# Optimization experiments

Measured on AMD Instinct MI355X. Metric: run time of the kernel, lower is better.

## Reference

```python
import jax, jax.numpy as jnp
import numpy as np
from jax.ops import segment_sum, segment_max

N, E = 50000, 800000
IN_FEATS, H, D_HID, N_CLASSES = 256, 4, 32, 47
NEG_SLOPE = 0.2


def leaky_relu(x, slope=NEG_SLOPE):
    return jnp.where(x >= 0, x, slope * x)


def gat_conv(h, W, attn_l, attn_r, src, dst, n_nodes, heads, d_out):
    # h: [N, F_in]; W: [F_in, heads*d_out]; attn_l/attn_r: [heads, d_out]
    feat = (h @ W).reshape(n_nodes, heads, d_out)          # [N, H, D]
    el = jnp.sum(feat * attn_l, axis=-1)                   # [N, H]
    er = jnp.sum(feat * attn_r, axis=-1)                   # [N, H]
    e = leaky_relu(el[src] + er[dst])                      # [E, H]
    # segment softmax over incoming edges of each dst node
    e_max = segment_max(e, dst, num_segments=n_nodes)      # [N, H]
    e_exp = jnp.exp(e - e_max[dst])                        # [E, H]
    denom = segment_sum(e_exp, dst, num_segments=n_nodes)  # [N, H]
    alpha = e_exp / denom[dst]                             # [E, H]
    msg = feat[src] * alpha[..., None]                     # [E, H, D]
    return segment_sum(msg, dst, num_segments=n_nodes)     # [N, H, D]


def setup_inputs() -> dict:
    key = jax.random.key(0)
    ks = jax.random.split(key, 12)
    hd = H * D_HID
    def glorot(k, shape):
        fan = shape[0] + shape[-1] if len(shape) == 2 else int(np.prod(shape))
        return jax.random.normal(k, shape, dtype=jnp.float32) * np.sqrt(2.0 / fan)
    return {
        "x": jax.random.normal(ks[0], (N, IN_FEATS), dtype=jnp.float32),
        "src": jax.random.randint(ks[1], (E,), 0, N),
        "dst": jax.random.randint(ks[2], (E,), 0, N),
        "W1": glorot(ks[3], (IN_FEATS, hd)),
        "al1": glorot(ks[4], (H, D_HID)),
        "ar1": glorot(ks[5], (H, D_HID)),
        "W2": glorot(ks[6], (hd, hd)),
        "al2": glorot(ks[7], (H, D_HID)),
        "ar2": glorot(ks[8], (H, D_HID)),
        "W3": glorot(ks[9], (hd, H * N_CLASSES)),
        "al3": glorot(ks[10], (H, N_CLASSES)),
        "ar3": glorot(ks[11], (H, N_CLASSES)),
    }


def reference(x, src, dst, W1, al1, ar1, W2, al2, ar2, W3, al3, ar3):
    # layer 1: ELU activation, flatten heads
    h = gat_conv(x, W1, al1, ar1, src, dst, N, H, D_HID)
    h = jax.nn.elu(h).reshape(N, H * D_HID)
    # layer 2
    h = gat_conv(h, W2, al2, ar2, src, dst, N, H, D_HID)
    h = jax.nn.elu(h).reshape(N, H * D_HID)
    # layer 3: no activation, mean over heads, log softmax
    h = gat_conv(h, W3, al3, ar3, src, dst, N, H, N_CLASSES)
    h = h.mean(axis=1)                                      # [N, n_classes]
    return jax.nn.log_softmax(h, axis=-1)
```

## Files before the change

kernel.cpp:

```cpp
#include <hip/hip_runtime.h>
#include <hip/hip_bf16.h>
#include <math.h>
#include <string.h>

#define N_NODES 50000
#define N_EDGES 800000
#define NH 4

typedef unsigned int u32;
typedef unsigned short u16;
typedef __attribute__((ext_vector_type(8))) short bf16x8;
typedef __attribute__((ext_vector_type(4))) float f32x4;

__device__ __forceinline__ u32 pack_bf2(float a, float b) {
    __hip_bfloat162 h2 = __float22bfloat162_rn(make_float2(a, b));
    u32 r;
    memcpy(&r, &h2, 4);
    return r;
}
__device__ __forceinline__ float2 bf2_to_f2(u32 u) {
    return make_float2(__uint_as_float(u << 16), __uint_as_float(u & 0xffff0000u));
}
__device__ __forceinline__ short bf16r(float f) {
    __hip_bfloat16 h = __float2bfloat16(f);
    short s;
    memcpy(&s, &h, 2);
    return s;
}

__device__ __forceinline__ float wred_max(float v) {
#pragma unroll
    for (int o = 32; o > 0; o >>= 1) v = fmaxf(v, __shfl_xor(v, o));
    return v;
}
__device__ __forceinline__ float wred_sum(float v) {
#pragma unroll
    for (int o = 32; o > 0; o >>= 1) v += __shfl_xor(v, o);
    return v;
}


__global__ void k_hist(const int* __restrict__ dst, int* __restrict__ deg) {
    int i = blockIdx.x * 256 + threadIdx.x;
    if (i < N_EDGES) atomicAdd(&deg[dst[i]], 1);
}

__global__ __launch_bounds__(1024) void k_scan1(const int* __restrict__ deg,
                                                int* __restrict__ offs,
                                                int* __restrict__ bsum) {
    __shared__ int tmp[1024];
    int b = blockIdx.x, t = threadIdx.x;
    int i = b * 1024 + t;
    int v = (i < N_NODES) ? deg[i] : 0;
    tmp[t] = v;
    __syncthreads();
    for (int off = 1; off < 1024; off <<= 1) {
        int add = (t >= off) ? tmp[t - off] : 0;
        __syncthreads();
        tmp[t] += add;
        __syncthreads();
    }
    if (i < N_NODES) offs[i] = tmp[t] - v;
    if (t == 1023) bsum[b] = tmp[t];
}

__global__ void k_scan2(int* __restrict__ bsum, int nb) {
    if (blockIdx.x == 0 && threadIdx.x == 0) {
        int run = 0;
        for (int b = 0; b < nb; ++b) { int v = bsum[b]; bsum[b] = run; run += v; }
    }
}

__global__ __launch_bounds__(1024) void k_scan3(int* __restrict__ offs,
                                                const int* __restrict__ bsum,
                                                int* __restrict__ cursor) {
    int b = blockIdx.x, t = threadIdx.x;
    int i = b * 1024 + t;
    if (i < N_NODES) {
        int o = offs[i] + bsum[b];
        offs[i] = o;
        cursor[i] = o;
    }
    if (b == 0 && t == 0) offs[N_NODES] = N_EDGES;
}

__global__ void k_scatter(const int* __restrict__ src, const int* __restrict__ dst,
                          int* __restrict__ cursor, int* __restrict__ csrc) {
    int i = blockIdx.x * 256 + threadIdx.x;
    if (i < N_EDGES) {
        int p = atomicAdd(&cursor[dst[i]], 1);
        csrc[p] = src[i];
    }
}

template <int K, int NOUT, int NP>
__global__ void prep_w(const float* __restrict__ W, u16* __restrict__ Wp) {
    constexpr int NT = NP / 16;
    int idx = blockIdx.x * 256 + threadIdx.x;
    int total = (K / 32) * NT * 64 * 8;
    if (idx >= total) return;
    int j = idx & 7;
    int lane = (idx >> 3) & 63;
    int rest = idx >> 9;
    int nt = rest % NT;
    int kt = rest / NT;
    int k = kt * 32 + (lane >> 4) * 8 + j;
    int col = nt * 16 + (lane & 15);
    float v = (col < NOUT) ? W[(size_t)k * NOUT + col] : 0.f;
    Wp[idx] = (u16)bf16r(v);
}

template <int K>
__global__ void prep_w3(const float* __restrict__ W, u16* __restrict__ Wp) {
    constexpr int NT = 12;
    int idx = blockIdx.x * 256 + threadIdx.x;
    int total = (K / 32) * NT * 64 * 8;
    if (idx >= total) return;
    int j = idx & 7;
    int lane = (idx >> 3) & 63;
    int rest = idx >> 9;
    int nt = rest % NT;
    int kt = rest / NT;
    int k = kt * 32 + (lane >> 4) * 8 + j;
    int col = nt * 16 + (lane & 15);
    int h = col / 48, d = col % 48;
    float v = (d < 47) ? W[(size_t)k * 188 + h * 47 + d] : 0.f;
    Wp[idx] = (u16)bf16r(v);
}

template <int K, int NOUT, int NP, bool AF32, bool DOTS, bool HEADPAD>
__global__ __launch_bounds__(256) void gemm_mfma(const void* __restrict__ Av,
                                                 const u16* __restrict__ Wp,
                                                 u16* __restrict__ feat,
                                                 const float* __restrict__ al,
                                                 const float* __restrict__ ar,
                                                 float* __restrict__ el,
                                                 float* __restrict__ er) {
    constexpr int NT = NP / 16;
    constexpr int KT = K / 32;
    int w = threadIdx.x >> 6, l = threadIdx.x & 63;
    int tile_m0 = blockIdx.x * 64 + w * 16;
    int c15 = l & 15;
    int rowA = tile_m0 + c15;
    if (rowA >= N_NODES) rowA = N_NODES - 1;
    int g = l >> 4;

    f32x4 acc[NT];
#pragma unroll
    for (int nt = 0; nt < NT; ++nt) acc[nt] = (f32x4){0.f, 0.f, 0.f, 0.f};

    for (int kt = 0; kt < KT; ++kt) {
        bf16x8 a;
        if constexpr (AF32) {
            const float* ap = (const float*)Av + (size_t)rowA * K + kt * 32 + g * 8;
            float4 f0 = *reinterpret_cast<const float4*>(ap);
            float4 f1 = *reinterpret_cast<const float4*>(ap + 4);
            a[0] = bf16r(f0.x); a[1] = bf16r(f0.y); a[2] = bf16r(f0.z); a[3] = bf16r(f0.w);
            a[4] = bf16r(f1.x); a[5] = bf16r(f1.y); a[6] = bf16r(f1.z); a[7] = bf16r(f1.w);
        } else {
            a = *reinterpret_cast<const bf16x8*>((const u16*)Av + (size_t)rowA * K + kt * 32 + g * 8);
        }
        const u16* wp = Wp + ((size_t)kt * NT) * 512 + (size_t)l * 8;
#pragma unroll
        for (int nt = 0; nt < NT; ++nt) {
            bf16x8 b = *reinterpret_cast<const bf16x8*>(wp + nt * 512);
            acc[nt] = __builtin_amdgcn_mfma_f32_16x16x32_bf16(a, b, acc[nt], 0, 0, 0);
        }
    }

    int rowD0 = tile_m0 + g * 4;
#pragma unroll
    for (int nt = 0; nt < NT; ++nt) {
        int col = nt * 16 + c15;
#pragma unroll
        for (int r = 0; r < 4; ++r) {
            int row = rowD0 + r;
            if (row < N_NODES)
                feat[(size_t)row * NP + col] = (u16)bf16r(acc[nt][r]);
        }
    }

    if constexpr (DOTS) {
        float alv[NT], arv[NT];
#pragma unroll
        for (int nt = 0; nt < NT; ++nt) {
            if constexpr (HEADPAD) {
                int h = nt / 3, m = nt % 3;
                if (m == 2) {
                    alv[nt] = (c15 < 15) ? al[h * 47 + 32 + c15] : 0.f;
                    arv[nt] = (c15 < 15) ? ar[h * 47 + 32 + c15] : 0.f;
                } else {
                    alv[nt] = al[h * 47 + m * 16 + c15];
                    arv[nt] = ar[h * 47 + m * 16 + c15];
                }
            } else {
                alv[nt] = al[nt * 16 + c15];
                arv[nt] = ar[nt * 16 + c15];
            }
        }
#pragma unroll
        for (int r = 0; r < 4; ++r) {
            float hlv[NH] = {0.f, 0.f, 0.f, 0.f};
            float hrv[NH] = {0.f, 0.f, 0.f, 0.f};
#pragma unroll
            for (int nt = 0; nt < NT; ++nt) {
                constexpr int NTH = NT / NH;
                int h = nt / NTH;
                hlv[h] = fmaf(acc[nt][r], alv[nt], hlv[h]);
                hrv[h] = fmaf(acc[nt][r], arv[nt], hrv[h]);
            }
#pragma unroll
            for (int o = 1; o < 16; o <<= 1) {
#pragma unroll
                for (int j = 0; j < NH; ++j) {
                    hlv[j] += __shfl_xor(hlv[j], o);
                    hrv[j] += __shfl_xor(hrv[j], o);
                }
            }
            int row = rowD0 + r;
            if (c15 == 0 && row < N_NODES) {
                *reinterpret_cast<float4*>(el + (size_t)row * NH) =
                    make_float4(hlv[0], hlv[1], hlv[2], hlv[3]);
                *reinterpret_cast<float4*>(er + (size_t)row * NH) =
                    make_float4(hrv[0], hrv[1], hrv[2], hrv[3]);
            }
        }
    }
}

__device__ __forceinline__ void alpha_chunk_T(const float* __restrict__ el,
                                              const int* __restrict__ csrc,
                                              float4 erv, int base, int i1,
                                              float4 mref, float4 vinv, bool online,
                                              float* __restrict__ lalT,
                                              int* __restrict__ lsrc, int lane) {
    int e = base + lane;
    bool act = e < i1;
    int srcn = act ? csrc[e] : 0;
    float4 elv = make_float4(0.f, 0.f, 0.f, 0.f);
    if (act) elv = *reinterpret_cast<const float4*>(el + (size_t)srcn * NH);
    float e0 = elv.x + erv.x; e0 = e0 >= 0.f ? e0 : 0.2f * e0;
    float e1 = elv.y + erv.y; e1 = e1 >= 0.f ? e1 : 0.2f * e1;
    float e2 = elv.z + erv.z; e2 = e2 >= 0.f ? e2 : 0.2f * e2;
    float e3 = elv.w + erv.w; e3 = e3 >= 0.f ? e3 : 0.2f * e3;
    float4 a4;
    if (online) {
        const float NEG = -__builtin_inff();
        float f0 = act ? e0 : NEG, f1 = act ? e1 : NEG, f2 = act ? e2 : NEG, f3 = act ? e3 : NEG;
        float m0 = wred_max(f0), m1 = wred_max(f1), m2 = wred_max(f2), m3 = wred_max(f3);
        float p0 = act ? __expf(e0 - m0) : 0.f;
        float p1 = act ? __expf(e1 - m1) : 0.f;
        float p2 = act ? __expf(e2 - m2) : 0.f;
        float p3 = act ? __expf(e3 - m3) : 0.f;
        float s0 = wred_sum(p0), s1 = wred_sum(p1), s2 = wred_sum(p2), s3 = wred_sum(p3);
        a4 = make_float4(act ? p0 / s0 : 0.f, act ? p1 / s1 : 0.f,
                         act ? p2 / s2 : 0.f, act ? p3 / s3 : 0.f);
    } else {
        a4 = make_float4(act ? __expf(e0 - mref.x) * vinv.x : 0.f,
                         act ? __expf(e1 - mref.y) * vinv.y : 0.f,
                         act ? __expf(e2 - mref.z) * vinv.z : 0.f,
                         act ? __expf(e3 - mref.w) * vinv.w : 0.f);
    }
    lalT[0 * 64 + lane] = a4.x;
    lalT[1 * 64 + lane] = a4.y;
    lalT[2 * 64 + lane] = a4.z;
    lalT[3 * 64 + lane] = a4.w;
    lsrc[lane] = srcn;
}

__device__ __forceinline__ void stats_pass(const float* __restrict__ el,
                                           const int* __restrict__ csrc,
                                           float4 erv, int i0, int i1, int lane,
                                           float4& mout, float4& vout) {
    const float NEG = -__builtin_inff();
    float m0 = NEG, m1 = NEG, m2 = NEG, m3 = NEG;
    float s0 = 0.f, s1 = 0.f, s2 = 0.f, s3 = 0.f;
    for (int base = i0; base < i1; base += 64) {
        int i = base + lane;
        bool act = i < i1;
        int srcn = act ? csrc[i] : 0;
        float4 elv = make_float4(0.f, 0.f, 0.f, 0.f);
        if (act) elv = *reinterpret_cast<const float4*>(el + (size_t)srcn * NH);
        float e0 = elv.x + erv.x; e0 = e0 >= 0.f ? e0 : 0.2f * e0;
        float e1 = elv.y + erv.y; e1 = e1 >= 0.f ? e1 : 0.2f * e1;
        float e2 = elv.z + erv.z; e2 = e2 >= 0.f ? e2 : 0.2f * e2;
        float e3 = elv.w + erv.w; e3 = e3 >= 0.f ? e3 : 0.2f * e3;
        if (!act) { e0 = NEG; e1 = NEG; e2 = NEG; e3 = NEG; }
        float c0 = wred_max(e0), c1 = wred_max(e1), c2 = wred_max(e2), c3 = wred_max(e3);
        float nm0 = fmaxf(m0, c0), nm1 = fmaxf(m1, c1), nm2 = fmaxf(m2, c2), nm3 = fmaxf(m3, c3);
        float p0 = act ? __expf(e0 - nm0) : 0.f;
        float p1 = act ? __expf(e1 - nm1) : 0.f;
        float p2 = act ? __expf(e2 - nm2) : 0.f;
        float p3 = act ? __expf(e3 - nm3) : 0.f;
        float S0 = wred_sum(p0), S1 = wred_sum(p1), S2 = wred_sum(p2), S3 = wred_sum(p3);
        s0 = s0 * __expf(m0 - nm0) + S0; m0 = nm0;
        s1 = s1 * __expf(m1 - nm1) + S1; m1 = nm1;
        s2 = s2 * __expf(m2 - nm2) + S2; m2 = nm2;
        s3 = s3 * __expf(m3 - nm3) + S3; m3 = nm3;
    }
    mout = make_float4(m0, m1, m2, m3);
    vout = make_float4(1.f / s0, 1.f / s1, 1.f / s2, 1.f / s3);
}

__global__ __launch_bounds__(256) void gat_agg128(const u16* __restrict__ feat,
                                                  const float* __restrict__ el,
                                                  const float* __restrict__ er,
                                                  const int* __restrict__ offs,
                                                  const int* __restrict__ csrc,
                                                  u16* __restrict__ out) {
    __shared__ float lalT[4][4][64];
    __shared__ int lsrc[4][64];
    int wave = threadIdx.x >> 6;
    int lane = threadIdx.x & 63;
    int n = blockIdx.x * 4 + wave;
    int h = lane >> 4;
    int i0 = offs[n], i1 = offs[n + 1];
    int d = i1 - i0;
    float ax = 0.f, ay = 0.f;
    if (d > 0) {
        float4 erv = *reinterpret_cast<const float4*>(er + (size_t)n * NH);
        float4 mref = make_float4(0.f, 0.f, 0.f, 0.f), vinv = mref;
        bool onechunk = d <= 64;
        if (!onechunk) stats_pass(el, csrc, erv, i0, i1, lane, mref, vinv);
        for (int base = i0; base < i1; base += 64) {
            alpha_chunk_T(el, csrc, erv, base, i1, mref, vinv, onechunk,
                          &lalT[wave][0][0], &lsrc[wave][0], lane);
            int cnt = i1 - base; if (cnt > 64) cnt = 64;
            int cpad = (cnt + 3) & ~3;
            for (int j = 0; j < cpad; j += 4) {
                int4 sv = *reinterpret_cast<const int4*>(&lsrc[wave][j]);
                float4 aq = *reinterpret_cast<const float4*>(&lalT[wave][h][j]);
                u32 q0 = *reinterpret_cast<const u32*>(feat + (size_t)sv.x * 128 + 2 * lane);
                u32 q1 = *reinterpret_cast<const u32*>(feat + (size_t)sv.y * 128 + 2 * lane);
                u32 q2 = *reinterpret_cast<const u32*>(feat + (size_t)sv.z * 128 + 2 * lane);
                u32 q3 = *reinterpret_cast<const u32*>(feat + (size_t)sv.w * 128 + 2 * lane);
                float2 v;
                v = bf2_to_f2(q0); ax = fmaf(aq.x, v.x, ax); ay = fmaf(aq.x, v.y, ay);
                v = bf2_to_f2(q1); ax = fmaf(aq.y, v.x, ax); ay = fmaf(aq.y, v.y, ay);
                v = bf2_to_f2(q2); ax = fmaf(aq.z, v.x, ax); ay = fmaf(aq.z, v.y, ay);
                v = bf2_to_f2(q3); ax = fmaf(aq.w, v.x, ax); ay = fmaf(aq.w, v.y, ay);
            }
        }
    }
    float ox = ax > 0.f ? ax : expm1f(ax);
    float oy = ay > 0.f ? ay : expm1f(ay);
    *reinterpret_cast<u32*>(out + (size_t)n * 128 + 2 * lane) = pack_bf2(ox, oy);
}

__global__ __launch_bounds__(256) void gat_agg_final(const u16* __restrict__ feat,
                                                     const float* __restrict__ el,
                                                     const float* __restrict__ er,
                                                     const int* __restrict__ offs,
                                                     const int* __restrict__ csrc,
                                                     float* __restrict__ out) {
    __shared__ float lalT[4][4][64];
    __shared__ int lsrc[4][64];
    __shared__ float lds[4][192];
    int wave = threadIdx.x >> 6;
    int lane = threadIdx.x & 63;
    int n = blockIdx.x * 4 + wave;
    int e0 = 2 * lane;
    bool up = lane < 32;
    int hLo = e0 / 48;
    int hHi = up ? (128 + e0) / 48 : 3;
    int i0 = offs[n], i1 = offs[n + 1];
    int d = i1 - i0;
    float a00 = 0.f, a01 = 0.f, a10 = 0.f, a11 = 0.f;
    if (d > 0) {
        float4 erv = *reinterpret_cast<const float4*>(er + (size_t)n * NH);
        float4 mref = make_float4(0.f, 0.f, 0.f, 0.f), vinv = mref;
        bool onechunk = d <= 64;
        if (!onechunk) stats_pass(el, csrc, erv, i0, i1, lane, mref, vinv);
        for (int base = i0; base < i1; base += 64) {
            alpha_chunk_T(el, csrc, erv, base, i1, mref, vinv, onechunk,
                          &lalT[wave][0][0], &lsrc[wave][0], lane);
            int cnt = i1 - base; if (cnt > 64) cnt = 64;
            int cpad = (cnt + 3) & ~3;
            for (int j = 0; j < cpad; j += 4) {
                int4 sv = *reinterpret_cast<const int4*>(&lsrc[wave][j]);
                float4 wlo = *reinterpret_cast<const float4*>(&lalT[wave][hLo][j]);
                float4 whi = *reinterpret_cast<const float4*>(&lalT[wave][hHi][j]);
                const u16* rA = feat + (size_t)sv.x * 192;
                const u16* rB = feat + (size_t)sv.y * 192;
                const u16* rC = feat + (size_t)sv.z * 192;
                const u16* rD = feat + (size_t)sv.w * 192;
                u32 a0 = *reinterpret_cast<const u32*>(rA + e0);
                u32 b0 = *reinterpret_cast<const u32*>(rB + e0);
                u32 c0 = *reinterpret_cast<const u32*>(rC + e0);
                u32 d0 = *reinterpret_cast<const u32*>(rD + e0);
                u32 a1 = up ? *reinterpret_cast<const u32*>(rA + 128 + e0) : 0u;
                u32 b1 = up ? *reinterpret_cast<const u32*>(rB + 128 + e0) : 0u;
                u32 c1 = up ? *reinterpret_cast<const u32*>(rC + 128 + e0) : 0u;
                u32 d1 = up ? *reinterpret_cast<const u32*>(rD + 128 + e0) : 0u;
                float2 v;
                v = bf2_to_f2(a0); a00 = fmaf(wlo.x, v.x, a00); a01 = fmaf(wlo.x, v.y, a01);
                v = bf2_to_f2(b0); a00 = fmaf(wlo.y, v.x, a00); a01 = fmaf(wlo.y, v.y, a01);
                v = bf2_to_f2(c0); a00 = fmaf(wlo.z, v.x, a00); a01 = fmaf(wlo.z, v.y, a01);
                v = bf2_to_f2(d0); a00 = fmaf(wlo.w, v.x, a00); a01 = fmaf(wlo.w, v.y, a01);
                v = bf2_to_f2(a1); a10 = fmaf(whi.x, v.x, a10); a11 = fmaf(whi.x, v.y, a11);
                v = bf2_to_f2(b1); a10 = fmaf(whi.y, v.x, a10); a11 = fmaf(whi.y, v.y, a11);
                v = bf2_to_f2(c1); a10 = fmaf(whi.z, v.x, a10); a11 = fmaf(whi.z, v.y, a11);
                v = bf2_to_f2(d1); a10 = fmaf(whi.w, v.x, a10); a11 = fmaf(whi.w, v.y, a11);
            }
        }
    }
    lds[wave][e0] = a00;
    lds[wave][e0 + 1] = a01;
    if (up) {
        lds[wave][128 + e0] = a10;
        lds[wave][129 + e0] = a11;
    }
    __syncthreads();
    float u = (lane < 47)
                  ? 0.25f * (lds[wave][lane] + lds[wave][48 + lane] +
                             lds[wave][96 + lane] + lds[wave][144 + lane])
                  : -__builtin_inff();
    float mx = u;
#pragma unroll
    for (int o = 32; o > 0; o >>= 1) mx = fmaxf(mx, __shfl_xor(mx, o));
    float ex = (lane < 47) ? __expf(u - mx) : 0.f;
    float sm = ex;
#pragma unroll
    for (int o = 32; o > 0; o >>= 1) sm += __shfl_xor(sm, o);
    if (lane < 47) out[(size_t)n * 47 + lane] = u - mx - logf(sm);
}


extern "C" void kernel_launch(void* const* d_in, const int* in_sizes, int n_in,
                              void* d_out, int out_size, void* d_ws, size_t ws_size,
                              hipStream_t stream) {
    const float* x = (const float*)d_in[0];
    const int* src = (const int*)d_in[1];
    const int* dst = (const int*)d_in[2];
    const float* W1 = (const float*)d_in[3];
    const float* al1 = (const float*)d_in[4];
    const float* ar1 = (const float*)d_in[5];
    const float* W2 = (const float*)d_in[6];
    const float* al2 = (const float*)d_in[7];
    const float* ar2 = (const float*)d_in[8];
    const float* W3 = (const float*)d_in[9];
    const float* al3 = (const float*)d_in[10];
    const float* ar3 = (const float*)d_in[11];
    float* out = (float*)d_out;

    char* p = (char*)d_ws;
    auto alloc = [&](size_t bytes) {
        char* r = p;
        p += (bytes + 255) & ~(size_t)255;
        return r;
    };
    u16* bufA = (u16*)alloc((size_t)N_NODES * 128 * 2);
    u16* bufC = (u16*)alloc((size_t)N_NODES * 128 * 2);
    u16* featb = (u16*)alloc((size_t)N_NODES * 192 * 2);
    float* el = (float*)alloc((size_t)N_NODES * NH * 4);
    float* er = (float*)alloc((size_t)N_NODES * NH * 4);
    u16* wp1 = (u16*)alloc((size_t)(256 / 32) * 8 * 512 * 2);
    u16* wp2 = (u16*)alloc((size_t)(128 / 32) * 8 * 512 * 2);
    u16* wp3 = (u16*)alloc((size_t)(128 / 32) * 12 * 512 * 2);
    int* deg = (int*)alloc((size_t)N_NODES * 4);
    int* offs = (int*)alloc((size_t)(N_NODES + 1) * 4);
    int* cursor = (int*)alloc((size_t)N_NODES * 4);
    int* bsum = (int*)alloc(64 * 4);
    int* csrc = (int*)alloc((size_t)N_EDGES * 4);

    prep_w<256, 128, 128><<<(8 * 8 * 512 + 255) / 256, 256, 0, stream>>>(W1, wp1);
    prep_w<128, 128, 128><<<(4 * 8 * 512 + 255) / 256, 256, 0, stream>>>(W2, wp2);
    prep_w3<128><<<(4 * 12 * 512 + 255) / 256, 256, 0, stream>>>(W3, wp3);

    hipMemsetAsync(deg, 0, (size_t)N_NODES * 4, stream);
    k_hist<<<(N_EDGES + 255) / 256, 256, 0, stream>>>(dst, deg);
    k_scan1<<<49, 1024, 0, stream>>>(deg, offs, bsum);
    k_scan2<<<1, 64, 0, stream>>>(bsum, 49);
    k_scan3<<<49, 1024, 0, stream>>>(offs, bsum, cursor);
    k_scatter<<<(N_EDGES + 255) / 256, 256, 0, stream>>>(src, dst, cursor, csrc);

    int gemm_grid = (N_NODES + 63) / 64;
    gemm_mfma<256, 128, 128, true, true, false><<<gemm_grid, 256, 0, stream>>>(x, wp1, featb, al1, ar1, el, er);
    gat_agg128<<<N_NODES / 4, 256, 0, stream>>>(featb, el, er, offs, csrc, bufA);
    gemm_mfma<128, 128, 128, false, true, false><<<gemm_grid, 256, 0, stream>>>(bufA, wp2, featb, al2, ar2, el, er);
    gat_agg128<<<N_NODES / 4, 256, 0, stream>>>(featb, el, er, offs, csrc, bufC);
    gemm_mfma<128, 192, 192, false, true, true><<<gemm_grid, 256, 0, stream>>>(bufC, wp3, featb, al3, ar3, el, er);
    gat_agg_final<<<N_NODES / 4, 256, 0, stream>>>(featb, el, er, offs, csrc, out);
}
```

Measured before the change: 314.1 us.

## Merge weight-prep kernels, warp-scan block sums, and use packed FMA in aggregation

Merges the three weight-packing kernels into a single launch and replaces the serial single-thread block-sum scan with a wavefront shuffle scan. The aggregation kernels now store each attention weight twice in a padded LDS layout, so v_pk_fma_f32 can apply one weight to both bf16-unpacked feature lanes at once. The goal is fewer launches, a shorter serial scan, and half as many FMA instructions in the gather loops. In exchange, LDS attention reads double and inline asm may limit compiler scheduling.

Measured after the change: 302.8 us. 3.6% less time.

```diff
diff --git a/kernel.cpp b/kernel.cpp
--- a/kernel.cpp
+++ b/kernel.cpp
@@ -6,11 +6,13 @@
 #define N_NODES 50000
 #define N_EDGES 800000
 #define NH 4
+#define LSTR 136
 
 typedef unsigned int u32;
 typedef unsigned short u16;
 typedef __attribute__((ext_vector_type(8))) short bf16x8;
 typedef __attribute__((ext_vector_type(4))) float f32x4;
+typedef __attribute__((ext_vector_type(2))) float f32x2;
 
 __device__ __forceinline__ u32 pack_bf2(float a, float b) {
     __hip_bfloat162 h2 = __float22bfloat162_rn(make_float2(a, b));
@@ -18,14 +20,20 @@
     memcpy(&r, &h2, 4);
     return r;
 }
-__device__ __forceinline__ float2 bf2_to_f2(u32 u) {
-    return make_float2(__uint_as_float(u << 16), __uint_as_float(u & 0xffff0000u));
+__device__ __forceinline__ f32x2 bf2_to_v2(u32 u) {
+    f32x2 v;
+    v.x = __uint_as_float(u << 16);
+    v.y = __uint_as_float(u & 0xffff0000u);
+    return v;
 }
 __device__ __forceinline__ short bf16r(float f) {
     __hip_bfloat16 h = __float2bfloat16(f);
     short s;
     memcpy(&s, &h, 2);
     return s;
+}
+__device__ __forceinline__ void pkfma(f32x2& acc, f32x2 a, f32x2 b) {
+    asm("v_pk_fma_f32 %0, %1, %2, %0" : "+v"(acc) : "v"(a), "v"(b));
 }
 
 __device__ __forceinline__ float wred_max(float v) {
@@ -65,10 +73,15 @@
 }
 
 __global__ void k_scan2(int* __restrict__ bsum, int nb) {
-    if (blockIdx.x == 0 && threadIdx.x == 0) {
-        int run = 0;
-        for (int b = 0; b < nb; ++b) { int v = bsum[b]; bsum[b] = run; run += v; }
-    }
+    int t = threadIdx.x & 63;
+    int v = (t < nb) ? bsum[t] : 0;
+    int orig = v;
+#pragma unroll
+    for (int o = 1; o < 64; o <<= 1) {
+        int u = __shfl_up(v, o);
+        if (t >= o) v += u;
+    }
+    if (t < nb) bsum[t] = v - orig;
 }
 
 __global__ __launch_bounds__(1024) void k_scan3(int* __restrict__ offs,
@@ -93,39 +106,42 @@
     }
 }
 
-template <int K, int NOUT, int NP>
-__global__ void prep_w(const float* __restrict__ W, u16* __restrict__ Wp) {
-    constexpr int NT = NP / 16;
-    int idx = blockIdx.x * 256 + threadIdx.x;
-    int total = (K / 32) * NT * 64 * 8;
-    if (idx >= total) return;
-    int j = idx & 7;
-    int lane = (idx >> 3) & 63;
-    int rest = idx >> 9;
+__device__ __forceinline__ u16 pack_elem(const float* W, int i, int K, int NT, int NOUT) {
+    int j = i & 7;
+    int lane = (i >> 3) & 63;
+    int rest = i >> 9;
     int nt = rest % NT;
     int kt = rest / NT;
     int k = kt * 32 + (lane >> 4) * 8 + j;
     int col = nt * 16 + (lane & 15);
     float v = (col < NOUT) ? W[(size_t)k * NOUT + col] : 0.f;
-    Wp[idx] = (u16)bf16r(v);
-}
-
-template <int K>
-__global__ void prep_w3(const float* __restrict__ W, u16* __restrict__ Wp) {
-    constexpr int NT = 12;
-    int idx = blockIdx.x * 256 + threadIdx.x;
-    int total = (K / 32) * NT * 64 * 8;
-    if (idx >= total) return;
-    int j = idx & 7;
-    int lane = (idx >> 3) & 63;
-    int rest = idx >> 9;
-    int nt = rest % NT;
-    int kt = rest / NT;
+    return (u16)bf16r(v);
+}
+__device__ __forceinline__ u16 pack_elem3(const float* W, int i) {
+    int j = i & 7;
+    int lane = (i >> 3) & 63;
+    int rest = i >> 9;
+    int nt = rest % 12;
+    int kt = rest / 12;
     int k = kt * 32 + (lane >> 4) * 8 + j;
     int col = nt * 16 + (lane & 15);
     int h = col / 48, d = col % 48;
     float v = (d < 47) ? W[(size_t)k * 188 + h * 47 + d] : 0.f;
-    Wp[idx] = (u16)bf16r(v);
+    return (u16)bf16r(v);
+}
+__global__ void prep_all(const float* __restrict__ W1, const float* __restrict__ W2,
+                         const float* __restrict__ W3, u16* __restrict__ wp1,
+                         u16* __restrict__ wp2, u16* __restrict__ wp3) {
+    int idx = blockIdx.x * 256 + threadIdx.x;
+    if (idx < 32768) {
+        wp1[idx] = pack_elem(W1, idx, 256, 8, 128);
+    } else if (idx < 49152) {
+        int i = idx - 32768;
+        wp2[i] = pack_elem(W2, i, 128, 8, 128);
+    } else if (idx < 73728) {
+        int i = idx - 49152;
+        wp3[i] = pack_elem3(W3, i);
+    }
 }
 
 template <int K, int NOUT, int NP, bool AF32, bool DOTS, bool HEADPAD>
@@ -261,10 +277,10 @@
                          act ? __expf(e2 - mref.z) * vinv.z : 0.f,
                          act ? __expf(e3 - mref.w) * vinv.w : 0.f);
     }
-    lalT[0 * 64 + lane] = a4.x;
-    lalT[1 * 64 + lane] = a4.y;
-    lalT[2 * 64 + lane] = a4.z;
-    lalT[3 * 64 + lane] = a4.w;
+    *reinterpret_cast<f32x2*>(&lalT[0 * LSTR + 2 * lane]) = (f32x2){a4.x, a4.x};
+    *reinterpret_cast<f32x2*>(&lalT[1 * LSTR + 2 * lane]) = (f32x2){a4.y, a4.y};
+    *reinterpret_cast<f32x2*>(&lalT[2 * LSTR + 2 * lane]) = (f32x2){a4.z, a4.z};
+    *reinterpret_cast<f32x2*>(&lalT[3 * LSTR + 2 * lane]) = (f32x2){a4.w, a4.w};
     lsrc[lane] = srcn;
 }
 
@@ -308,7 +324,7 @@
                                                   const int* __restrict__ offs,
                                                   const int* __restrict__ csrc,
                                                   u16* __restrict__ out) {
-    __shared__ float lalT[4][4][64];
+    __shared__ float lalT[4][4][LSTR];
     __shared__ int lsrc[4][64];
     int wave = threadIdx.x >> 6;
     int lane = threadIdx.x & 63;
@@ -316,7 +332,7 @@
     int h = lane >> 4;
     int i0 = offs[n], i1 = offs[n + 1];
     int d = i1 - i0;
-    float ax = 0.f, ay = 0.f;
+    f32x2 acc = (f32x2){0.f, 0.f};
     if (d > 0) {
         float4 erv = *reinterpret_cast<const float4*>(er + (size_t)n * NH);
         float4 mref = make_float4(0.f, 0.f, 0.f, 0.f), vinv = mref;
@@ -329,21 +345,25 @@
             int cpad = (cnt + 3) & ~3;
             for (int j = 0; j < cpad; j += 4) {
                 int4 sv = *reinterpret_cast<const int4*>(&lsrc[wave][j]);
-                float4 aq = *reinterpret_cast<const float4*>(&lalT[wave][h][j]);
-                u32 q0 = *reinterpret_cast<const u32*>(feat + (size_t)sv.x * 128 + 2 * lane);
-                u32 q1 = *reinterpret_cast<const u32*>(feat + (size_t)sv.y * 128 + 2 * lane);
-                u32 q2 = *reinterpret_cast<const u32*>(feat + (size_t)sv.z * 128 + 2 * lane);
-                u32 q3 = *reinterpret_cast<const u32*>(feat + (size_t)sv.w * 128 + 2 * lane);
-                float2 v;
-                v = bf2_to_f2(q0); ax = fmaf(aq.x, v.x, ax); ay = fmaf(aq.x, v.y, ay);
-                v = bf2_to_f2(q1); ax = fmaf(aq.y, v.x, ax); ay = fmaf(aq.y, v.y, ay);
-                v = bf2_to_f2(q2); ax = fmaf(aq.z, v.x, ax); ay = fmaf(aq.z, v.y, ay);
-                v = bf2_to_f2(q3); ax = fmaf(aq.w, v.x, ax); ay = fmaf(aq.w, v.y, ay);
+                float4 q01 = *reinterpret_cast<const float4*>(&lalT[wave][h][2 * j]);
+                float4 q23 = *reinterpret_cast<const float4*>(&lalT[wave][h][2 * j + 4]);
+                u32 u0 = *reinterpret_cast<const u32*>(feat + (size_t)sv.x * 128 + 2 * lane);
+                u32 u1 = *reinterpret_cast<const u32*>(feat + (size_t)sv.y * 128 + 2 * lane);
+                u32 u2 = *reinterpret_cast<const u32*>(feat + (size_t)sv.z * 128 + 2 * lane);
+                u32 u3 = *reinterpret_cast<const u32*>(feat + (size_t)sv.w * 128 + 2 * lane);
+                f32x2 a0 = __builtin_shufflevector(*(const f32x4*)&q01, *(const f32x4*)&q01, 0, 1);
+                f32x2 a1 = __builtin_shufflevector(*(const f32x4*)&q01, *(const f32x4*)&q01, 2, 3);
+                f32x2 a2 = __builtin_shufflevector(*(const f32x4*)&q23, *(const f32x4*)&q23, 0, 1);
+                f32x2 a3 = __builtin_shufflevector(*(const f32x4*)&q23, *(const f32x4*)&q23, 2, 3);
+                pkfma(acc, a0, bf2_to_v2(u0));
+                pkfma(acc, a1, bf2_to_v2(u1));
+                pkfma(acc, a2, bf2_to_v2(u2));
+                pkfma(acc, a3, bf2_to_v2(u3));
             }
         }
     }
-    float ox = ax > 0.f ? ax : expm1f(ax);
-    float oy = ay > 0.f ? ay : expm1f(ay);
+    float ox = acc.x > 0.f ? acc.x : expm1f(acc.x);
+    float oy = acc.y > 0.f ? acc.y : expm1f(acc.y);
     *reinterpret_cast<u32*>(out + (size_t)n * 128 + 2 * lane) = pack_bf2(ox, oy);
 }
 
@@ -353,7 +373,7 @@
                                                      const int* __restrict__ offs,
                                                      const int* __restrict__ csrc,
                                                      float* __restrict__ out) {
-    __shared__ float lalT[4][4][64];
+    __shared__ float lalT[4][4][LSTR];
     __shared__ int lsrc[4][64];
     __shared__ float lds[4][192];
     int wave = threadIdx.x >> 6;
@@ -365,7 +385,8 @@
     int hHi = up ? (128 + e0) / 48 : 3;
     int i0 = offs[n], i1 = offs[n + 1];
     int d = i1 - i0;
-    float a00 = 0.f, a01 = 0.f, a10 = 0.f, a11 = 0.f;
+    f32x2 accLo = (f32x2){0.f, 0.f};
+    f32x2 accHi = (f32x2){0.f, 0.f};
     if (d > 0) {
         float4 erv = *reinterpret_cast<const float4*>(er + (size_t)n * NH);
         float4 mref = make_float4(0.f, 0.f, 0.f, 0.f), vinv = mref;
@@ -378,8 +399,10 @@
             int cpad = (cnt + 3) & ~3;
             for (int j = 0; j < cpad; j += 4) {
                 int4 sv = *reinterpret_cast<const int4*>(&lsrc[wave][j]);
-                float4 wlo = *reinterpret_cast<const float4*>(&lalT[wave][hLo][j]);
-                float4 whi = *reinterpret_cast<const float4*>(&lalT[wave][hHi][j]);
+                float4 lo01 = *reinterpret_cast<const float4*>(&lalT[wave][hLo][2 * j]);
+                float4 lo23 = *reinterpret_cast<const float4*>(&lalT[wave][hLo][2 * j + 4]);
+                float4 hi01 = *reinterpret_cast<const float4*>(&lalT[wave][hHi][2 * j]);
+                float4 hi23 = *reinterpret_cast<const float4*>(&lalT[wave][hHi][2 * j + 4]);
                 const u16* rA = feat + (size_t)sv.x * 192;
                 const u16* rB = feat + (size_t)sv.y * 192;
                 const u16* rC = feat + (size_t)sv.z * 192;
@@ -392,23 +415,30 @@
                 u32 b1 = up ? *reinterpret_cast<const u32*>(rB + 128 + e0) : 0u;
                 u32 c1 = up ? *reinterpret_cast<const u32*>(rC + 128 + e0) : 0u;
                 u32 d1 = up ? *reinterpret_cast<const u32*>(rD + 128 + e0) : 0u;
-                float2 v;
-                v = bf2_to_f2(a0); a00 = fmaf(wlo.x, v.x, a00); a01 = fmaf(wlo.x, v.y, a01);
-                v = bf2_to_f2(b0); a00 = fmaf(wlo.y, v.x, a00); a01 = fmaf(wlo.y, v.y, a01);
-                v = bf2_to_f2(c0); a00 = fmaf(wlo.z, v.x, a00); a01 = fmaf(wlo.z, v.y, a01);
-                v = bf2_to_f2(d0); a00 = fmaf(wlo.w, v.x, a00); a01 = fmaf(wlo.w, v.y, a01);
-                v = bf2_to_f2(a1); a10 = fmaf(whi.x, v.x, a10); a11 = fmaf(whi.x, v.y, a11);
-                v = bf2_to_f2(b1); a10 = fmaf(whi.y, v.x, a10); a11 = fmaf(whi.y, v.y, a11);
-                v = bf2_to_f2(c1); a10 = fmaf(whi.z, v.x, a10); a11 = fmaf(whi.z, v.y, a11);
-                v = bf2_to_f2(d1); a10 = fmaf(whi.w, v.x, a10); a11 = fmaf(whi.w, v.y, a11);
+                f32x2 wA = __builtin_shufflevector(*(const f32x4*)&lo01, *(const f32x4*)&lo01, 0, 1);
+                f32x2 wB = __builtin_shufflevector(*(const f32x4*)&lo01, *(const f32x4*)&lo01, 2, 3);
+                f32x2 wC = __builtin_shufflevector(*(const f32x4*)&lo23, *(const f32x4*)&lo23, 0, 1);
+                f32x2 wD = __builtin_shufflevector(*(const f32x4*)&lo23, *(const f32x4*)&lo23, 2, 3);
+                pkfma(accLo, wA, bf2_to_v2(a0));
+                pkfma(accLo, wB, bf2_to_v2(b0));
+                pkfma(accLo, wC, bf2_to_v2(c0));
+                pkfma(accLo, wD, bf2_to_v2(d0));
+                f32x2 vA = __builtin_shufflevector(*(const f32x4*)&hi01, *(const f32x4*)&hi01, 0, 1);
+                f32x2 vB = __builtin_shufflevector(*(const f32x4*)&hi01, *(const f32x4*)&hi01, 2, 3);
+                f32x2 vC = __builtin_shufflevector(*(const f32x4*)&hi23, *(const f32x4*)&hi23, 0, 1);
+                f32x2 vD = __builtin_shufflevector(*(const f32x4*)&hi23, *(const f32x4*)&hi23, 2, 3);
+                pkfma(accHi, vA, bf2_to_v2(a1));
+                pkfma(accHi, vB, bf2_to_v2(b1));
+                pkfma(accHi, vC, bf2_to_v2(c1));
+                pkfma(accHi, vD, bf2_to_v2(d1));
             }
         }
     }
-    lds[wave][e0] = a00;
-    lds[wave][e0 + 1] = a01;
+    lds[wave][e0] = accLo.x;
+    lds[wave][e0 + 1] = accLo.y;
     if (up) {
-        lds[wave][128 + e0] = a10;
-        lds[wave][129 + e0] = a11;
+        lds[wave][128 + e0] = accHi.x;
+        lds[wave][129 + e0] = accHi.y;
     }
     __syncthreads();
     float u = (lane < 47)
@@ -454,18 +484,16 @@
     u16* featb = (u16*)alloc((size_t)N_NODES * 192 * 2);
     float* el = (float*)alloc((size_t)N_NODES * NH * 4);
     float* er = (float*)alloc((size_t)N_NODES * NH * 4);
-    u16* wp1 = (u16*)alloc((size_t)(256 / 32) * 8 * 512 * 2);
-    u16* wp2 = (u16*)alloc((size_t)(128 / 32) * 8 * 512 * 2);
-    u16* wp3 = (u16*)alloc((size_t)(128 / 32) * 12 * 512 * 2);
+    u16* wp1 = (u16*)alloc((size_t)32768 * 2);
+    u16* wp2 = (u16*)alloc((size_t)16384 * 2);
+    u16* wp3 = (u16*)alloc((size_t)24576 * 2);
     int* deg = (int*)alloc((size_t)N_NODES * 4);
     int* offs = (int*)alloc((size_t)(N_NODES + 1) * 4);
     int* cursor = (int*)alloc((size_t)N_NODES * 4);
     int* bsum = (int*)alloc(64 * 4);
     int* csrc = (int*)alloc((size_t)N_EDGES * 4);
 
-    prep_w<256, 128, 128><<<(8 * 8 * 512 + 255) / 256, 256, 0, stream>>>(W1, wp1);
-    prep_w<128, 128, 128><<<(4 * 8 * 512 + 255) / 256, 256, 0, stream>>>(W2, wp2);
-    prep_w3<128><<<(4 * 12 * 512 + 255) / 256, 256, 0, stream>>>(W3, wp3);
+    prep_all<<<288, 256, 0, stream>>>(W1, W2, W3, wp1, wp2, wp3);
 
     hipMemsetAsync(deg, 0, (size_t)N_NODES * 4, stream);
     k_hist<<<(N_EDGES + 255) / 256, 256, 0, stream>>>(dst, deg);
```

## Merge weight-prep kernels, parallelize block scan, pad LDS, use 32-bit gather offsets

Applied to the files above, without the earlier changes.

Merges the three weight-packing kernels into one launch, which removes two kernel launches. Replaces the single-thread serial block-sum scan with a wave-level shuffle scan. Pads the transposed alpha LDS rows to a stride of 68 so the layout differs from a plain power-of-two stride. Computes feature gather addresses as 32-bit byte offsets instead of 64-bit pointer arithmetic, which may save address instructions in the aggregation loops. All of these are small overhead trims around the main memory-bound gather.

After: 292.0 us. 7.0% less time.

```diff
diff --git a/kernel.cpp b/kernel.cpp
--- a/kernel.cpp
+++ b/kernel.cpp
@@ -6,6 +6,7 @@
 #define N_NODES 50000
 #define N_EDGES 800000
 #define NH 4
+#define LSTR 68
 
 typedef unsigned int u32;
 typedef unsigned short u16;
@@ -65,10 +66,15 @@
 }
 
 __global__ void k_scan2(int* __restrict__ bsum, int nb) {
-    if (blockIdx.x == 0 && threadIdx.x == 0) {
-        int run = 0;
-        for (int b = 0; b < nb; ++b) { int v = bsum[b]; bsum[b] = run; run += v; }
-    }
+    int t = threadIdx.x & 63;
+    int v = (t < nb) ? bsum[t] : 0;
+    int orig = v;
+#pragma unroll
+    for (int o = 1; o < 64; o <<= 1) {
+        int u = __shfl_up(v, o);
+        if (t >= o) v += u;
+    }
+    if (t < nb) bsum[t] = v - orig;
 }
 
 __global__ __launch_bounds__(1024) void k_scan3(int* __restrict__ offs,
@@ -93,39 +99,42 @@
     }
 }
 
-template <int K, int NOUT, int NP>
-__global__ void prep_w(const float* __restrict__ W, u16* __restrict__ Wp) {
-    constexpr int NT = NP / 16;
-    int idx = blockIdx.x * 256 + threadIdx.x;
-    int total = (K / 32) * NT * 64 * 8;
-    if (idx >= total) return;
-    int j = idx & 7;
-    int lane = (idx >> 3) & 63;
-    int rest = idx >> 9;
+__device__ __forceinline__ u16 pack_elem(const float* W, int i, int K, int NT, int NOUT) {
+    int j = i & 7;
+    int lane = (i >> 3) & 63;
+    int rest = i >> 9;
     int nt = rest % NT;
     int kt = rest / NT;
     int k = kt * 32 + (lane >> 4) * 8 + j;
     int col = nt * 16 + (lane & 15);
     float v = (col < NOUT) ? W[(size_t)k * NOUT + col] : 0.f;
-    Wp[idx] = (u16)bf16r(v);
-}
-
-template <int K>
-__global__ void prep_w3(const float* __restrict__ W, u16* __restrict__ Wp) {
-    constexpr int NT = 12;
-    int idx = blockIdx.x * 256 + threadIdx.x;
-    int total = (K / 32) * NT * 64 * 8;
-    if (idx >= total) return;
-    int j = idx & 7;
-    int lane = (idx >> 3) & 63;
-    int rest = idx >> 9;
-    int nt = rest % NT;
-    int kt = rest / NT;
+    return (u16)bf16r(v);
+}
+__device__ __forceinline__ u16 pack_elem3(const float* W, int i) {
+    int j = i & 7;
+    int lane = (i >> 3) & 63;
+    int rest = i >> 9;
+    int nt = rest % 12;
+    int kt = rest / 12;
     int k = kt * 32 + (lane >> 4) * 8 + j;
     int col = nt * 16 + (lane & 15);
     int h = col / 48, d = col % 48;
     float v = (d < 47) ? W[(size_t)k * 188 + h * 47 + d] : 0.f;
-    Wp[idx] = (u16)bf16r(v);
+    return (u16)bf16r(v);
+}
+__global__ void prep_all(const float* __restrict__ W1, const float* __restrict__ W2,
+                         const float* __restrict__ W3, u16* __restrict__ wp1,
+                         u16* __restrict__ wp2, u16* __restrict__ wp3) {
+    int idx = blockIdx.x * 256 + threadIdx.x;
+    if (idx < 32768) {
+        wp1[idx] = pack_elem(W1, idx, 256, 8, 128);
+    } else if (idx < 49152) {
+        int i = idx - 32768;
+        wp2[i] = pack_elem(W2, i, 128, 8, 128);
+    } else if (idx < 73728) {
+        int i = idx - 49152;
+        wp3[i] = pack_elem3(W3, i);
+    }
 }
 
 template <int K, int NOUT, int NP, bool AF32, bool DOTS, bool HEADPAD>
@@ -261,10 +270,10 @@
                          act ? __expf(e2 - mref.z) * vinv.z : 0.f,
                          act ? __expf(e3 - mref.w) * vinv.w : 0.f);
     }
-    lalT[0 * 64 + lane] = a4.x;
-    lalT[1 * 64 + lane] = a4.y;
-    lalT[2 * 64 + lane] = a4.z;
-    lalT[3 * 64 + lane] = a4.w;
+    lalT[0 * LSTR + lane] = a4.x;
+    lalT[1 * LSTR + lane] = a4.y;
+    lalT[2 * LSTR + lane] = a4.z;
+    lalT[3 * LSTR + lane] = a4.w;
     lsrc[lane] = srcn;
 }
 
@@ -308,12 +317,13 @@
                                                   const int* __restrict__ offs,
                                                   const int* __restrict__ csrc,
                                                   u16* __restrict__ out) {
-    __shared__ float lalT[4][4][64];
+    __shared__ float lalT[4][4][LSTR];
     __shared__ int lsrc[4][64];
     int wave = threadIdx.x >> 6;
     int lane = threadIdx.x & 63;
     int n = blockIdx.x * 4 + wave;
     int h = lane >> 4;
+    u32 lo4 = (u32)lane * 4u;
     int i0 = offs[n], i1 = offs[n + 1];
     int d = i1 - i0;
     float ax = 0.f, ay = 0.f;
@@ -322,6 +332,7 @@
         float4 mref = make_float4(0.f, 0.f, 0.f, 0.f), vinv = mref;
         bool onechunk = d <= 64;
         if (!onechunk) stats_pass(el, csrc, erv, i0, i1, lane, mref, vinv);
+        const char* fbase = (const char*)feat;
         for (int base = i0; base < i1; base += 64) {
             alpha_chunk_T(el, csrc, erv, base, i1, mref, vinv, onechunk,
                           &lalT[wave][0][0], &lsrc[wave][0], lane);
@@ -330,10 +341,14 @@
             for (int j = 0; j < cpad; j += 4) {
                 int4 sv = *reinterpret_cast<const int4*>(&lsrc[wave][j]);
                 float4 aq = *reinterpret_cast<const float4*>(&lalT[wave][h][j]);
-                u32 q0 = *reinterpret_cast<const u32*>(feat + (size_t)sv.x * 128 + 2 * lane);
-                u32 q1 = *reinterpret_cast<const u32*>(feat + (size_t)sv.y * 128 + 2 * lane);
-                u32 q2 = *reinterpret_cast<const u32*>(feat + (size_t)sv.z * 128 + 2 * lane);
-                u32 q3 = *reinterpret_cast<const u32*>(feat + (size_t)sv.w * 128 + 2 * lane);
+                u32 o0 = ((u32)sv.x << 8) + lo4;
+                u32 o1 = ((u32)sv.y << 8) + lo4;
+                u32 o2 = ((u32)sv.z << 8) + lo4;
+                u32 o3 = ((u32)sv.w << 8) + lo4;
+                u32 q0 = *reinterpret_cast<const u32*>(fbase + o0);
+                u32 q1 = *reinterpret_cast<const u32*>(fbase + o1);
+                u32 q2 = *reinterpret_cast<const u32*>(fbase + o2);
+                u32 q3 = *reinterpret_cast<const u32*>(fbase + o3);
                 float2 v;
                 v = bf2_to_f2(q0); ax = fmaf(aq.x, v.x, ax); ay = fmaf(aq.x, v.y, ay);
                 v = bf2_to_f2(q1); ax = fmaf(aq.y, v.x, ax); ay = fmaf(aq.y, v.y, ay);
@@ -353,7 +368,7 @@
                                                      const int* __restrict__ offs,
                                                      const int* __restrict__ csrc,
                                                      float* __restrict__ out) {
-    __shared__ float lalT[4][4][64];
+    __shared__ float lalT[4][4][LSTR];
     __shared__ int lsrc[4][64];
     __shared__ float lds[4][192];
     int wave = threadIdx.x >> 6;
@@ -363,6 +378,7 @@
     bool up = lane < 32;
     int hLo = e0 / 48;
     int hHi = up ? (128 + e0) / 48 : 3;
+    u32 lo4 = (u32)lane * 4u;
     int i0 = offs[n], i1 = offs[n + 1];
     int d = i1 - i0;
     float a00 = 0.f, a01 = 0.f, a10 = 0.f, a11 = 0.f;
@@ -371,6 +387,7 @@
         float4 mref = make_float4(0.f, 0.f, 0.f, 0.f), vinv = mref;
         bool onechunk = d <= 64;
         if (!onechunk) stats_pass(el, csrc, erv, i0, i1, lane, mref, vinv);
+        const char* fbase = (const char*)feat;
         for (int base = i0; base < i1; base += 64) {
             alpha_chunk_T(el, csrc, erv, base, i1, mref, vinv, onechunk,
                           &lalT[wave][0][0], &lsrc[wave][0], lane);
@@ -380,18 +397,18 @@
                 int4 sv = *reinterpret_cast<const int4*>(&lsrc[wave][j]);
                 float4 wlo = *reinterpret_cast<const float4*>(&lalT[wave][hLo][j]);
                 float4 whi = *reinterpret_cast<const float4*>(&lalT[wave][hHi][j]);
-                const u16* rA = feat + (size_t)sv.x * 192;
-                const u16* rB = feat + (size_t)sv.y * 192;
-                const u16* rC = feat + (size_t)sv.z * 192;
-                const u16* rD = feat + (size_t)sv.w * 192;
-                u32 a0 = *reinterpret_cast<const u32*>(rA + e0);
-                u32 b0 = *reinterpret_cast<const u32*>(rB + e0);
-                u32 c0 = *reinterpret_cast<const u32*>(rC + e0);
-                u32 d0 = *reinterpret_cast<const u32*>(rD + e0);
-                u32 a1 = up ? *reinterpret_cast<const u32*>(rA + 128 + e0) : 0u;
-                u32 b1 = up ? *reinterpret_cast<const u32*>(rB + 128 + e0) : 0u;
-                u32 c1 = up ? *reinterpret_cast<const u32*>(rC + 128 + e0) : 0u;
-                u32 d1 = up ? *reinterpret_cast<const u32*>(rD + 128 + e0) : 0u;
+                u32 oA = (u32)sv.x * 384u + lo4;
+                u32 oB = (u32)sv.y * 384u + lo4;
+                u32 oC = (u32)sv.z * 384u + lo4;
+                u32 oD = (u32)sv.w * 384u + lo4;
+                u32 a0 = *reinterpret_cast<const u32*>(fbase + oA);
+                u32 b0 = *reinterpret_cast<const u32*>(fbase + oB);
+                u32 c0 = *reinterpret_cast<const u32*>(fbase + oC);
+                u32 d0 = *reinterpret_cast<const u32*>(fbase + oD);
+                u32 a1 = up ? *reinterpret_cast<const u32*>(fbase + oA + 256) : 0u;
+                u32 b1 = up ? *reinterpret_cast<const u32*>(fbase + oB + 256) : 0u;
+                u32 c1 = up ? *reinterpret_cast<const u32*>(fbase + oC + 256) : 0u;
+                u32 d1 = up ? *reinterpret_cast<const u32*>(fbase + oD + 256) : 0u;
                 float2 v;
                 v = bf2_to_f2(a0); a00 = fmaf(wlo.x, v.x, a00); a01 = fmaf(wlo.x, v.y, a01);
                 v = bf2_to_f2(b0); a00 = fmaf(wlo.y, v.x, a00); a01 = fmaf(wlo.y, v.y, a01);
@@ -454,18 +471,16 @@
     u16* featb = (u16*)alloc((size_t)N_NODES * 192 * 2);
     float* el = (float*)alloc((size_t)N_NODES * NH * 4);
     float* er = (float*)alloc((size_t)N_NODES * NH * 4);
-    u16* wp1 = (u16*)alloc((size_t)(256 / 32) * 8 * 512 * 2);
-    u16* wp2 = (u16*)alloc((size_t)(128 / 32) * 8 * 512 * 2);
-    u16* wp3 = (u16*)alloc((size_t)(128 / 32) * 12 * 512 * 2);
+    u16* wp1 = (u16*)alloc((size_t)32768 * 2);
+    u16* wp2 = (u16*)alloc((size_t)16384 * 2);
+    u16* wp3 = (u16*)alloc((size_t)24576 * 2);
     int* deg = (int*)alloc((size_t)N_NODES * 4);
     int* offs = (int*)alloc((size_t)(N_NODES + 1) * 4);
     int* cursor = (int*)alloc((size_t)N_NODES * 4);
     int* bsum = (int*)alloc(64 * 4);
     int* csrc = (int*)alloc((size_t)N_EDGES * 4);
 
-    prep_w<256, 128, 128><<<(8 * 8 * 512 + 255) / 256, 256, 0, stream>>>(W1, wp1);
-    prep_w<128, 128, 128><<<(4 * 8 * 512 + 255) / 256, 256, 0, stream>>>(W2, wp2);
-    prep_w3<128><<<(4 * 12 * 512 + 255) / 256, 256, 0, stream>>>(W3, wp3);
+    prep_all<<<288, 256, 0, stream>>>(W1, W2, W3, wp1, wp2, wp3);
 
     hipMemsetAsync(deg, 0, (size_t)N_NODES * 4, stream);
     k_hist<<<(N_EDGES + 255) / 256, 256, 0, stream>>>(dst, deg);
```
